# Performance work log

Measured on AMD Instinct MI355X. Metric: run time of the kernel, lower is better.

The kernel has to match this reference:

```python
import jax, jax.numpy as jnp
import numpy as np


def setup_inputs() -> dict:
    key = jax.random.key(0)
    k1, k2, k3 = jax.random.split(key, 3)
    N = 50000
    E = 1600000
    D = 128
    indices = jax.random.randint(k1, (2, E), 0, N, dtype=jnp.int64)
    values = jax.random.uniform(k2, (E,), dtype=jnp.float32)
    b = jax.random.normal(k3, (N, D), dtype=jnp.float32)
    return {"indices": indices, "values": values, "n": N, "b": b}


def reference(indices, values, n, b):
    # out = A @ b where A is sparse COO: A[row[e], col[e]] = values[e]
    rows = indices[0]  # [E]
    cols = indices[1]  # [E]
    # gather source features per edge, scale by edge value, scatter-add to rows
    contrib = values[:, None] * b[cols]  # [E, D]
    out = jax.ops.segment_sum(contrib, rows, num_segments=n)  # [N, D]
    return out
```

## Files before the change

### kernel.cpp

```cpp
#include <hip/hip_runtime.h>
#include <hip/hip_bf16.h>


#define D_DIM 128
#define CSX   16
#define SPILL_CAP (1 << 16)

__device__ inline uint f32_to_bf16(float f) {
    uint u = __float_as_uint(f);
    return (u + 0x7fffu + ((u >> 16) & 1u)) >> 16;
}

__global__ __launch_bounds__(256) void cvt_kernel(const float* __restrict__ b,
                                                  ushort* __restrict__ b16, int n8) {
    int i = blockIdx.x * 256 + threadIdx.x;
    int stride = gridDim.x * 256;
    for (; i < n8; i += stride) {
        float4 f0 = *reinterpret_cast<const float4*>(b + (size_t)i * 8);
        float4 f1 = *reinterpret_cast<const float4*>(b + (size_t)i * 8 + 4);
        uint r[8] = {f32_to_bf16(f0.x), f32_to_bf16(f0.y),
                     f32_to_bf16(f0.z), f32_to_bf16(f0.w),
                     f32_to_bf16(f1.x), f32_to_bf16(f1.y),
                     f32_to_bf16(f1.z), f32_to_bf16(f1.w)};
        uint4 w;
        w.x = r[0] | (r[1] << 16);
        w.y = r[2] | (r[3] << 16);
        w.z = r[4] | (r[5] << 16);
        w.w = r[6] | (r[7] << 16);
        *reinterpret_cast<uint4*>(b16 + (size_t)i * 8) = w;
    }
}

__global__ __launch_bounds__(256) void scatter_x(const int* __restrict__ rows,
                                                 const int* __restrict__ cols,
                                                 const float* __restrict__ vals,
                                                 int* __restrict__ rowcnt,
                                                 int* __restrict__ spill_cnt,
                                                 int2* __restrict__ spill,
                                                 uint* __restrict__ slots,
                                                 int E, int N) {
    const int  t = threadIdx.x;
    const int  x = blockIdx.x & 7;
    int*  cntx  = rowcnt + (size_t)x * N;
    uint* slotx = slots + (size_t)x * N * CSX;
    long e0 = (long)blockIdx.x * 1024 + t * 4;
    if (e0 + 3 < E) {
        int4   r4 = *reinterpret_cast<const int4*>(rows + e0);
        int4   c4 = *reinterpret_cast<const int4*>(cols + e0);
        float4 v4 = *reinterpret_cast<const float4*>(vals + e0);
        int   rr[4] = {r4.x, r4.y, r4.z, r4.w};
        int   cc[4] = {c4.x, c4.y, c4.z, c4.w};
        float vv[4] = {v4.x, v4.y, v4.z, v4.w};
        #pragma unroll
        for (int k = 0; k < 4; ++k) {
            int pos = atomicAdd(&cntx[rr[k]], 1);
            uint w  = ((uint)cc[k] << 16) | f32_to_bf16(vv[k]);
            if (pos < CSX) {
                slotx[(size_t)rr[k] * CSX + pos] = w;
            } else {
                int sp = atomicAdd(spill_cnt, 1);
                if (sp < SPILL_CAP)
                    spill[sp] = make_int2((rr[k] << 16) | cc[k], __float_as_int(vv[k]));
            }
        }
    } else {
        for (int k = 0; k < 4; ++k) {
            long e = e0 + k;
            if (e >= E) break;
            int r = rows[e], c = cols[e];
            float v = vals[e];
            int pos = atomicAdd(&cntx[r], 1);
            uint w  = ((uint)c << 16) | f32_to_bf16(v);
            if (pos < CSX) {
                slotx[(size_t)r * CSX + pos] = w;
            } else {
                int sp = atomicAdd(spill_cnt, 1);
                if (sp < SPILL_CAP)
                    spill[sp] = make_int2((r << 16) | c, __float_as_int(v));
            }
        }
    }
}

__device__ inline void bf16_fma4(float4& acc, float v, uint2 u) {
    float f0 = __uint_as_float(u.x << 16);
    float f1 = __uint_as_float(u.x & 0xffff0000u);
    float f2 = __uint_as_float(u.y << 16);
    float f3 = __uint_as_float(u.y & 0xffff0000u);
    acc.x = fmaf(v, f0, acc.x);
    acc.y = fmaf(v, f1, acc.y);
    acc.z = fmaf(v, f2, acc.z);
    acc.w = fmaf(v, f3, acc.w);
}

__global__ __launch_bounds__(256) void reduce_x(const int* __restrict__ rowcnt,
                                                const uint* __restrict__ slots,
                                                const ushort* __restrict__ b16,
                                                float* __restrict__ out, int N) {
    __shared__ uint sbuf[4][8 * CSX];
    const int w    = threadIdx.x >> 6;
    const int lane = threadIdx.x & 63;
    const int half = lane >> 5;
    const int l32  = lane & 31;
    const int row  = blockIdx.x * 4 + w;
    if (row >= N) return;

    int tot = 0;
    #pragma unroll
    for (int x = 0; x < 8; ++x) {
        int cx = __builtin_amdgcn_readfirstlane(rowcnt[(size_t)x * N + row]);
        if (cx > CSX) cx = CSX;
        if (lane < cx)
            sbuf[w][tot + lane] = slots[((size_t)x * N + row) * CSX + lane];
        tot += cx;
    }

    const ushort* bl = b16 + l32 * 4;
    float4 acc = make_float4(0.f, 0.f, 0.f, 0.f);
    int j = 0;
    for (; j + 16 <= tot; j += 16) {
        uint uu[8];
        #pragma unroll
        for (int k = 0; k < 8; ++k) uu[k] = sbuf[w][j + 2 * k + half];
        uint2 bv[8];
        #pragma unroll
        for (int k = 0; k < 8; ++k)
            bv[k] = *reinterpret_cast<const uint2*>(bl + (size_t)(uu[k] >> 16) * D_DIM);
        #pragma unroll
        for (int k = 0; k < 8; ++k)
            bf16_fma4(acc, __uint_as_float(uu[k] << 16), bv[k]);
    }
    for (; j + 4 <= tot; j += 4) {
        uint u0 = sbuf[w][j + half];
        uint u1 = sbuf[w][j + 2 + half];
        uint2 b0 = *reinterpret_cast<const uint2*>(bl + (size_t)(u0 >> 16) * D_DIM);
        uint2 b1 = *reinterpret_cast<const uint2*>(bl + (size_t)(u1 >> 16) * D_DIM);
        bf16_fma4(acc, __uint_as_float(u0 << 16), b0);
        bf16_fma4(acc, __uint_as_float(u1 << 16), b1);
    }
    for (; j + 2 <= tot; j += 2) {
        uint u = sbuf[w][j + half];
        uint2 bb = *reinterpret_cast<const uint2*>(bl + (size_t)(u >> 16) * D_DIM);
        bf16_fma4(acc, __uint_as_float(u << 16), bb);
    }
    if (j < tot) {
        uint u = sbuf[w][j];
        uint  c = half ? 0u : (u >> 16);
        float v = half ? 0.f : __uint_as_float(u << 16);
        uint2 bb = *reinterpret_cast<const uint2*>(bl + (size_t)c * D_DIM);
        bf16_fma4(acc, v, bb);
    }
    acc.x += __shfl_xor(acc.x, 32, 64);
    acc.y += __shfl_xor(acc.y, 32, 64);
    acc.z += __shfl_xor(acc.z, 32, 64);
    acc.w += __shfl_xor(acc.w, 32, 64);
    if (half == 0)
        *reinterpret_cast<float4*>(out + (size_t)row * D_DIM + l32 * 4) = acc;
}

__global__ __launch_bounds__(256) void spill_apply(const int2* __restrict__ spill,
                                                   const int* __restrict__ spill_cnt,
                                                   const float* __restrict__ b,
                                                   float* __restrict__ out) {
    int total = *spill_cnt;
    if (total > SPILL_CAP) total = SPILL_CAP;
    const int lane  = threadIdx.x & 63;
    const int wid   = (blockIdx.x * 256 + threadIdx.x) >> 6;
    const int nwave = (gridDim.x * 256) >> 6;
    for (int i = wid; i < total; i += nwave) {
        int2 a = spill[i];
        int r = (int)((unsigned)a.x >> 16);
        int c = a.x & 0xffff;
        float v = __int_as_float(a.y);
        float2 bb = *reinterpret_cast<const float2*>(b + (size_t)c * D_DIM + lane * 2);
        atomicAdd(&out[(size_t)r * D_DIM + lane * 2],     v * bb.x);
        atomicAdd(&out[(size_t)r * D_DIM + lane * 2 + 1], v * bb.y);
    }
}

__global__ __launch_bounds__(256) void zero_kernel(float* __restrict__ out, size_t n4) {
    size_t i = (size_t)blockIdx.x * 256 + threadIdx.x;
    size_t stride = (size_t)gridDim.x * 256;
    for (; i < n4; i += stride)
        reinterpret_cast<float4*>(out)[i] = make_float4(0.f, 0.f, 0.f, 0.f);
}

__global__ __launch_bounds__(256) void atomic_spmm_kernel(const int* __restrict__ rows,
                                                          const int* __restrict__ cols,
                                                          const float* __restrict__ vals,
                                                          const float* __restrict__ b,
                                                          float* __restrict__ out, int E) {
    long long t = (long long)blockIdx.x * 256 + threadIdx.x;
    int e = (int)(t >> 5);
    int q = (int)(t & 31);
    if (e >= E) return;
    int   r = rows[e];
    int   c = cols[e];
    float v = vals[e];
    float4 bb = *reinterpret_cast<const float4*>(b + (size_t)c * D_DIM + q * 4);
    float* o = out + (size_t)r * D_DIM + q * 4;
    atomicAdd(o + 0, v * bb.x);
    atomicAdd(o + 1, v * bb.y);
    atomicAdd(o + 2, v * bb.z);
    atomicAdd(o + 3, v * bb.w);
}

extern "C" void kernel_launch(void* const* d_in, const int* in_sizes, int n_in,
                              void* d_out, int out_size, void* d_ws, size_t ws_size,
                              hipStream_t stream) {
    const int*   idx  = (const int*)d_in[0];
    const float* vals = (const float*)d_in[1];
    const float* b    = (const float*)d_in[3];
    float*       out  = (float*)d_out;

    const int E = in_sizes[1];
    const int N = in_sizes[3] / D_DIM;
    const int* rows = idx;
    const int* cols = idx + E;

    size_t spill_off = (((size_t)(8 * (size_t)N + 1) * sizeof(int)) + 15) & ~(size_t)15;
    size_t slots_off = spill_off + (size_t)SPILL_CAP * sizeof(int2);
    size_t b16_off   = slots_off + 8 * (size_t)N * CSX * sizeof(uint);
    size_t need      = b16_off + (size_t)N * D_DIM * sizeof(ushort);

    if (ws_size >= need && N <= 65536) {
        char*   ws        = (char*)d_ws;
        int*    rowcnt    = (int*)ws;
        int*    spill_cnt = rowcnt + 8 * (size_t)N;
        int2*   spill     = (int2*)(ws + spill_off);
        uint*   slots     = (uint*)(ws + slots_off);
        ushort* b16       = (ushort*)(ws + b16_off);

        hipMemsetAsync(rowcnt, 0, (8 * (size_t)N + 1) * sizeof(int), stream);
        cvt_kernel<<<2048, 256, 0, stream>>>(b, b16, N * D_DIM / 8);
        int sb = (int)((E + 1023) / 1024);
        scatter_x<<<sb, 256, 0, stream>>>(rows, cols, vals, rowcnt,
                                          spill_cnt, spill, slots, E, N);
        reduce_x<<<(N + 3) / 4, 256, 0, stream>>>(rowcnt, slots, b16, out, N);
        spill_apply<<<64, 256, 0, stream>>>(spill, spill_cnt, b, out);
    } else {
        size_t n4 = (size_t)N * D_DIM / 4;
        zero_kernel<<<2048, 256, 0, stream>>>(out, n4);
        long long total = (long long)E * 32;
        int ab = (int)((total + 255) / 256);
        atomic_spmm_kernel<<<ab, 256, 0, stream>>>(rows, cols, vals, b, out, E);
    }
}
```

Measured before the change: 273.2 us.

## Fuse bf16 conversion into scatter kernel and pick slot copy by hardware XCC id

Merges the bf16 conversion kernel and the edge scatter kernel into one launch, with extra blocks past the scatter range doing the conversion, so the two independent stages overlap and one launch is removed. Each scatter block now chooses its per-XCC counter and slot copy from the hardware XCC_ID register instead of blockIdx&7, so atomics stay in the local XCC's L2. Edge arrays are read with nontemporal loads and workspace offsets are aligned to 64 bytes. The register read ties the code to MI300-class hardware.

```diff
diff --git a/kernel.cpp b/kernel.cpp
--- a/kernel.cpp
+++ b/kernel.cpp
@@ -5,49 +5,64 @@
 #define D_DIM 128
 #define CSX   16
 #define SPILL_CAP (1 << 16)
+#define CVTB  512
+
+typedef int   vint4   __attribute__((ext_vector_type(4)));
+typedef float vfloat4 __attribute__((ext_vector_type(4)));
 
 __device__ inline uint f32_to_bf16(float f) {
     uint u = __float_as_uint(f);
     return (u + 0x7fffu + ((u >> 16) & 1u)) >> 16;
 }
 
-__global__ __launch_bounds__(256) void cvt_kernel(const float* __restrict__ b,
-                                                  ushort* __restrict__ b16, int n8) {
-    int i = blockIdx.x * 256 + threadIdx.x;
-    int stride = gridDim.x * 256;
-    for (; i < n8; i += stride) {
-        float4 f0 = *reinterpret_cast<const float4*>(b + (size_t)i * 8);
-        float4 f1 = *reinterpret_cast<const float4*>(b + (size_t)i * 8 + 4);
-        uint r[8] = {f32_to_bf16(f0.x), f32_to_bf16(f0.y),
-                     f32_to_bf16(f0.z), f32_to_bf16(f0.w),
-                     f32_to_bf16(f1.x), f32_to_bf16(f1.y),
-                     f32_to_bf16(f1.z), f32_to_bf16(f1.w)};
-        uint4 w;
-        w.x = r[0] | (r[1] << 16);
-        w.y = r[2] | (r[3] << 16);
-        w.z = r[4] | (r[5] << 16);
-        w.w = r[6] | (r[7] << 16);
-        *reinterpret_cast<uint4*>(b16 + (size_t)i * 8) = w;
-    }
-}
-
-__global__ __launch_bounds__(256) void scatter_x(const int* __restrict__ rows,
-                                                 const int* __restrict__ cols,
-                                                 const float* __restrict__ vals,
-                                                 int* __restrict__ rowcnt,
-                                                 int* __restrict__ spill_cnt,
-                                                 int2* __restrict__ spill,
-                                                 uint* __restrict__ slots,
-                                                 int E, int N) {
-    const int  t = threadIdx.x;
-    const int  x = blockIdx.x & 7;
+__device__ inline int xcc_id() {
+    int x;
+    asm volatile("s_getreg_b32 %0, hwreg(HW_REG_XCC_ID)" : "=s"(x));
+    return x & 7;
+}
+
+__global__ __launch_bounds__(256) void cvt_scatter(const int* __restrict__ rows,
+                                                   const int* __restrict__ cols,
+                                                   const float* __restrict__ vals,
+                                                   const float* __restrict__ b,
+                                                   ushort* __restrict__ b16, int n8,
+                                                   int* __restrict__ rowcnt,
+                                                   int* __restrict__ spill_cnt,
+                                                   int2* __restrict__ spill,
+                                                   uint* __restrict__ slots,
+                                                   int E, int N, int SB) {
+    const int t = threadIdx.x;
+    if ((int)blockIdx.x >= SB) {
+        int i = ((int)blockIdx.x - SB) * 256 + t;
+        const int stride = CVTB * 256;
+        for (; i < n8; i += stride) {
+            float4 f0 = *reinterpret_cast<const float4*>(b + (size_t)i * 8);
+            float4 f1 = *reinterpret_cast<const float4*>(b + (size_t)i * 8 + 4);
+            uint r[8] = {f32_to_bf16(f0.x), f32_to_bf16(f0.y),
+                         f32_to_bf16(f0.z), f32_to_bf16(f0.w),
+                         f32_to_bf16(f1.x), f32_to_bf16(f1.y),
+                         f32_to_bf16(f1.z), f32_to_bf16(f1.w)};
+            uint4 w;
+            w.x = r[0] | (r[1] << 16);
+            w.y = r[2] | (r[3] << 16);
+            w.z = r[4] | (r[5] << 16);
+            w.w = r[6] | (r[7] << 16);
+            *reinterpret_cast<uint4*>(b16 + (size_t)i * 8) = w;
+        }
+        return;
+    }
+
+    const int x = xcc_id();
     int*  cntx  = rowcnt + (size_t)x * N;
     uint* slotx = slots + (size_t)x * N * CSX;
     long e0 = (long)blockIdx.x * 1024 + t * 4;
     if (e0 + 3 < E) {
-        int4   r4 = *reinterpret_cast<const int4*>(rows + e0);
-        int4   c4 = *reinterpret_cast<const int4*>(cols + e0);
-        float4 v4 = *reinterpret_cast<const float4*>(vals + e0);
+        vint4   r4 = __builtin_nontemporal_load(
+                         reinterpret_cast<const vint4*>(rows + e0));
+        vint4   c4 = __builtin_nontemporal_load(
+                         reinterpret_cast<const vint4*>(cols + e0));
+        vfloat4 v4 = __builtin_nontemporal_load(
+                         reinterpret_cast<const vfloat4*>(vals + e0));
         int   rr[4] = {r4.x, r4.y, r4.z, r4.w};
         int   cc[4] = {c4.x, c4.y, c4.z, c4.w};
         float vv[4] = {v4.x, v4.y, v4.z, v4.w};
@@ -218,8 +233,8 @@
     const int* rows = idx;
     const int* cols = idx + E;
 
-    size_t spill_off = (((size_t)(8 * (size_t)N + 1) * sizeof(int)) + 15) & ~(size_t)15;
-    size_t slots_off = spill_off + (size_t)SPILL_CAP * sizeof(int2);
+    size_t spill_off = (((size_t)(8 * (size_t)N + 1) * sizeof(int)) + 63) & ~(size_t)63;
+    size_t slots_off = (spill_off + (size_t)SPILL_CAP * sizeof(int2) + 63) & ~(size_t)63;
     size_t b16_off   = slots_off + 8 * (size_t)N * CSX * sizeof(uint);
     size_t need      = b16_off + (size_t)N * D_DIM * sizeof(ushort);
 
@@ -231,11 +246,12 @@
         uint*   slots     = (uint*)(ws + slots_off);
         ushort* b16       = (ushort*)(ws + b16_off);
 
-        hipMemsetAsync(rowcnt, 0, (8 * (size_t)N + 1) * sizeof(int), stream);
-        cvt_kernel<<<2048, 256, 0, stream>>>(b, b16, N * D_DIM / 8);
-        int sb = (int)((E + 1023) / 1024);
-        scatter_x<<<sb, 256, 0, stream>>>(rows, cols, vals, rowcnt,
-                                          spill_cnt, spill, slots, E, N);
+        (void)hipMemsetAsync(rowcnt, 0, (8 * (size_t)N + 1) * sizeof(int), stream);
+        const int SB = (int)((E + 1023) / 1024);
+        cvt_scatter<<<SB + CVTB, 256, 0, stream>>>(rows, cols, vals, b, b16,
+                                                   N * D_DIM / 8, rowcnt,
+                                                   spill_cnt, spill, slots,
+                                                   E, N, SB);
         reduce_x<<<(N + 3) / 4, 256, 0, stream>>>(rowcnt, slots, b16, out, N);
         spill_apply<<<64, 256, 0, stream>>>(spill, spill_cnt, b, out);
     } else {
```

Result: no change. 271.0 us (-0.8%).
